# Kernel optimization log

Hardware: AMD Instinct MI355X
Metric: run time of the kernel (lower is better)

The kernel has to match this reference:

```python
import jax, jax.numpy as jnp
import numpy as np

B, CQ, CKV, H, W = 4, 128, 256, 64, 64
NUM_HEADS = 8
SCALE = (CQ // NUM_HEADS) ** (-0.5)


def setup_inputs() -> dict:
    key = jax.random.key(0)
    ks = jax.random.split(key, 10)
    s = 0.02
    return {
        "x_q": jax.random.normal(ks[0], (B, CQ, H, W), dtype=jnp.float32),
        "x_kv": jax.random.normal(ks[1], (B, CKV, H, W), dtype=jnp.float32),
        "Wq": jax.random.normal(ks[2], (CQ, CQ), dtype=jnp.float32) * s,
        "bq": jnp.zeros((CQ,), dtype=jnp.float32),
        "Wk": jax.random.normal(ks[3], (CQ, CKV), dtype=jnp.float32) * s,
        "bk": jnp.zeros((CQ,), dtype=jnp.float32),
        "Wv": jax.random.normal(ks[4], (CQ, CKV), dtype=jnp.float32) * s,
        "bv": jnp.zeros((CQ,), dtype=jnp.float32),
        "Wo": jax.random.normal(ks[5], (CQ, CQ), dtype=jnp.float32) * s,
        "bo": jnp.zeros((CQ,), dtype=jnp.float32),
    }


def _conv1x1(x, Wm, bv_):
    # 1x1 conv == channel-mixing matmul: [B,C,H,W] x [O,C] -> [B,O,H,W]
    return jnp.einsum('bchw,oc->bohw', x, Wm) + bv_[:, None, None]


def reference(x_q, x_kv, Wq, bq, Wk, bk, Wv, bv, Wo, bo):
    b, c, h, w = x_q.shape
    n = h * w
    Q = _conv1x1(x_q, Wq, bq).reshape(b, c, n)   # [B,C,N]
    K = _conv1x1(x_kv, Wk, bk).reshape(b, c, n)  # [B,C,N]
    V = _conv1x1(x_kv, Wv, bv).reshape(b, c, n)  # [B,C,N]
    # attn = softmax(Q^T K * scale) over keys: [B,N,N]
    attn = jax.nn.softmax(jnp.einsum('bcn,bcm->bnm', Q, K) * SCALE, axis=-1)
    out = jnp.einsum('bnm,bcm->bcn', attn, V).reshape(b, c, h, w)
    out = _conv1x1(out, Wo, bo) + x_q
    return out
```

## Files before the change

kernel.cpp:

```cpp
#include <hip/hip_runtime.h>
#include <hip/hip_bf16.h>

typedef __bf16 bf16x8 __attribute__((ext_vector_type(8)));
typedef float f32x4 __attribute__((ext_vector_type(4)));
typedef float f32x16 __attribute__((ext_vector_type(16)));

#define MFMA16(a, b, c) __builtin_amdgcn_mfma_f32_16x16x32_bf16(a, b, c, 0, 0, 0)
#define MFMA32(a, b, c) __builtin_amdgcn_mfma_f32_32x32x16_bf16(a, b, c, 0, 0, 0)

static constexpr int NSP = 4096;
static constexpr float SCALE_L2E = 0.25f * 1.4426950408889634f;

__device__ __forceinline__ bf16x8 ld_frag(const void* p) {
  int4 v = *(const int4*)p;
  return __builtin_bit_cast(bf16x8, v);
}

__device__ __forceinline__ unsigned pk2(float a, float b) {
  unsigned short x = __builtin_bit_cast(unsigned short, (__bf16)a);
  unsigned short y = __builtin_bit_cast(unsigned short, (__bf16)b);
  return (unsigned)x | ((unsigned)y << 16);
}

__device__ __forceinline__ void load_lds16(const void* g, void* l) {
  __builtin_amdgcn_global_load_lds(
      (const __attribute__((address_space(1))) unsigned*)g,
      (__attribute__((address_space(3))) unsigned*)l, 16, 0, 0);
}

__global__ void k_prep(const float* __restrict__ Wq, const float* __restrict__ bq,
                       const float* __restrict__ Wk, const float* __restrict__ Wv,
                       const float* __restrict__ Wo,
                       __bf16* __restrict__ wqb, __bf16* __restrict__ wkb,
                       __bf16* __restrict__ wvb, __bf16* __restrict__ wob,
                       float* __restrict__ bqs) {
  int i = blockIdx.x * 256 + threadIdx.x;
  if (i < 16384)      wqb[i]          = (__bf16)(Wq[i] * SCALE_L2E);
  else if (i < 49152) wkb[i - 16384]  = (__bf16)Wk[i - 16384];
  else if (i < 81920) wvb[i - 49152]  = (__bf16)Wv[i - 49152];
  else if (i < 98304) wob[i - 81920]  = (__bf16)Wo[i - 81920];
  if (i < 128) bqs[i] = bq[i] * SCALE_L2E;
}

template <bool SWZ>
__device__ __forceinline__ void store_tile_T(char* myt, const f32x4* acc, int g, int r,
                                             __bf16* dst_base) {
#pragma unroll
  for (int oc = 0; oc < 8; ++oc) {
#pragma unroll
    for (int rr = 0; rr < 4; ++rr) {
      int o = oc * 16 + g * 4 + rr;
      int byte = (r << 8) + (((o << 1)) ^ (r << 4));
      *(__bf16*)(myt + byte) = (__bf16)acc[oc][rr];
    }
  }
  int l = g * 16 + r;
#pragma unroll
  for (int p = 0; p < 4; ++p) {
    int u = p * 64 + l, row = u >> 4, seg = u & 15;
    int byte = (row << 8) + (seg << 4);
    if (!SWZ) byte ^= (row & 15) << 4;
    int4 v = *(int4*)(myt + byte);
    *(int4*)(dst_base + row * 128 + seg * 8) = v;
  }
}

__global__ __launch_bounds__(256) void k_proj(const float* __restrict__ xq,
                                              const float* __restrict__ xkv,
                                              const __bf16* __restrict__ wqb,
                                              const __bf16* __restrict__ wkb,
                                              const __bf16* __restrict__ wvb,
                                              const float* __restrict__ bqs,
                                              const float* __restrict__ bk,
                                              const float* __restrict__ bv,
                                              __bf16* __restrict__ Qt,
                                              __bf16* __restrict__ Kt,
                                              __bf16* __restrict__ Vm) {
  const int t = threadIdx.x, w = t >> 6, l = t & 63, r = l & 15, g = l >> 4;
  __shared__ __align__(16) char lds[16384];
  char* myt = lds + (w << 12);

  if (blockIdx.x < 256) {
    const int b = blockIdx.x >> 6;
    const int n0 = (blockIdx.x & 63) << 6;
    const int nl = n0 + (w << 4) + r;
    const float* xb = xq + ((size_t)b << 19);
    bf16x8 bx[4];
#pragma unroll
    for (int cc = 0; cc < 4; ++cc) {
#pragma unroll
      for (int i = 0; i < 8; ++i) {
        int c = cc * 32 + g * 8 + i;
        bx[cc][i] = (__bf16)xb[c * 4096 + nl];
      }
    }
    f32x4 acc[8];
#pragma unroll
    for (int oc = 0; oc < 8; ++oc)
#pragma unroll
      for (int rr = 0; rr < 4; ++rr) acc[oc][rr] = bqs[oc * 16 + g * 4 + rr];
#pragma unroll
    for (int oc = 0; oc < 8; ++oc) {
#pragma unroll
      for (int cc = 0; cc < 4; ++cc) {
        bf16x8 a = ld_frag(wqb + (oc * 16 + r) * 128 + cc * 32 + g * 8);
        acc[oc] = MFMA16(a, bx[cc], acc[oc]);
      }
    }
    store_tile_T<false>(myt, acc, g, r, Qt + ((size_t)(b * NSP + n0 + w * 16)) * 128);
  } else {
    const int bid = blockIdx.x - 256;
    const int b = bid >> 6;
    const int n0 = (bid & 63) << 6;
    const int nl = n0 + (w << 4) + r;
    const float* xb = xkv + ((size_t)b << 20);
    bf16x8 bx[8];
#pragma unroll
    for (int cc = 0; cc < 8; ++cc) {
#pragma unroll
      for (int i = 0; i < 8; ++i) {
        int c = cc * 32 + g * 8 + i;
        bx[cc][i] = (__bf16)xb[(size_t)c * 4096 + nl];
      }
    }
    f32x4 acc[8];
#pragma unroll
    for (int oc = 0; oc < 8; ++oc)
#pragma unroll
      for (int rr = 0; rr < 4; ++rr) acc[oc][rr] = bk[oc * 16 + g * 4 + rr];
#pragma unroll
    for (int oc = 0; oc < 8; ++oc) {
#pragma unroll
      for (int cc = 0; cc < 8; ++cc) {
        bf16x8 a = ld_frag(wkb + (oc * 16 + r) * 256 + cc * 32 + g * 8);
        acc[oc] = MFMA16(a, bx[cc], acc[oc]);
      }
    }
    store_tile_T<true>(myt, acc, g, r, Kt + ((size_t)(b * NSP + n0 + w * 16)) * 128);

    f32x4 av[8];
#pragma unroll
    for (int oc = 0; oc < 8; ++oc)
#pragma unroll
      for (int rr = 0; rr < 4; ++rr) av[oc][rr] = bv[oc * 16 + g * 4 + rr];
#pragma unroll
    for (int oc = 0; oc < 8; ++oc) {
#pragma unroll
      for (int cc = 0; cc < 8; ++cc) {
        bf16x8 a = ld_frag(wvb + (oc * 16 + r) * 256 + cc * 32 + g * 8);
        av[oc] = MFMA16(a, bx[cc], av[oc]);
      }
    }
#pragma unroll
    for (int oc = 0; oc < 8; ++oc) {
#pragma unroll
      for (int rr = 0; rr < 4; ++rr) {
        int o = oc * 16 + g * 4 + rr;
        Vm[((size_t)(b * 128 + o) << 12) + (nl ^ ((o & 3) << 3))] = (__bf16)av[oc][rr];
      }
    }
  }
}

template <int SPLIT>
__global__ __launch_bounds__(256, 3) void k_flash(const __bf16* __restrict__ Qt,
                                                  const __bf16* __restrict__ Kt,
                                                  const __bf16* __restrict__ Vm,
                                                  __bf16* __restrict__ Op,
                                                  float2* __restrict__ Ml) {
  const int bid = blockIdx.x;
  const int combo = bid & (4 * SPLIT - 1), qtile = bid / (4 * SPLIT);
  const int b = combo & 3, ks = combo >> 2;
  const int q0 = qtile << 7;
  const int NK = NSP / SPLIT;
  const int t = threadIdx.x, w = t >> 6, l = t & 63;
  const int q31 = l & 31, hi = l >> 5;
  const int swz = (q31 & 15) << 4;
  const int swzV = (q31 & 3) << 4;

  __shared__ __align__(16) char kl[2][8192];
  __shared__ __align__(16) char vl[2][8192];

  const int qA = q0 + w * 32 + q31;
  const __bf16* qp = Qt + ((size_t)(b * NSP + qA)) * 128;
  bf16x8 qf[8];
#pragma unroll
  for (int cc = 0; cc < 8; ++cc) qf[cc] = ld_frag(qp + cc * 16 + hi * 8);

  f32x16 acc[4];
#pragma unroll
  for (int c = 0; c < 4; ++c)
#pragma unroll
    for (int i = 0; i < 16; ++i) acc[c][i] = 0.f;
  f32x4 lp = (f32x4){0.f, 0.f, 0.f, 0.f};

  const char* kbase = (const char*)(Kt + ((size_t)(b * NSP) + ks * NK) * 128);
  const char* vbase = (const char*)(Vm + (size_t)b * 128 * NSP + ks * NK);

  auto STAGE = [&](int bi, int tt) {
#pragma unroll
    for (int i = 0; i < 2; ++i) {
      int u = i * 256 + t;
      load_lds16(kbase + tt * 8192 + u * 16, &kl[bi][u * 16]);
    }
#pragma unroll
    for (int i = 0; i < 2; ++i) {
      int u = i * 256 + t, ch = u >> 2, ko = u & 3;
      load_lds16(vbase + (size_t)ch * 8192 + tt * 64 + ko * 16, &vl[bi][u * 16]);
    }
  };

  STAGE(0, 0);

  const int nit = NK / 32;
  for (int it = 0; it < nit; ++it) {
    const int cur = it & 1;
    asm volatile("s_barrier" ::: "memory");
    if (it + 1 < nit) {
      STAGE(cur ^ 1, it + 1);
      asm volatile("s_waitcnt vmcnt(4)" ::: "memory");
    } else {
      asm volatile("s_waitcnt vmcnt(0)" ::: "memory");
    }
    __builtin_amdgcn_sched_barrier(0);
    asm volatile("s_barrier" ::: "memory");

    const char* kt = kl[cur];
    f32x16 sX = {}, sY = {};
    __builtin_amdgcn_s_setprio(1);
#pragma unroll
    for (int cc = 0; cc < 4; ++cc) {
      bf16x8 kf0 = ld_frag(kt + (q31 << 8) + ((cc * 32 + hi * 16) ^ swz));
      bf16x8 kf1 = ld_frag(kt + (q31 << 8) + (((cc + 4) * 32 + hi * 16) ^ swz));
      sX = MFMA32(kf0, qf[cc], sX);
      sY = MFMA32(kf1, qf[cc + 4], sY);
    }
    __builtin_amdgcn_s_setprio(0);
    f32x16 s;
#pragma unroll
    for (int i = 0; i < 16; ++i) s[i] = sX[i] + sY[i];

#pragma unroll
    for (int i = 0; i < 16; ++i) s[i] = exp2f(s[i]);
#pragma unroll
    for (int i = 0; i < 16; ++i) lp[i & 3] += s[i];

    unsigned pA[4][2], rA[4][2];
#pragma unroll
    for (int q4 = 0; q4 < 4; ++q4) {
      pA[q4][0] = pk2(s[4 * q4 + 0], s[4 * q4 + 1]);
      pA[q4][1] = pk2(s[4 * q4 + 2], s[4 * q4 + 3]);
    }
#pragma unroll
    for (int q4 = 0; q4 < 4; ++q4) {
      rA[q4][0] = __shfl_xor(pA[q4][0], 32);
      rA[q4][1] = __shfl_xor(pA[q4][1], 32);
    }

    const char* vt = vl[cur];
    __builtin_amdgcn_s_setprio(1);
#pragma unroll
    for (int kb = 0; kb < 2; ++kb) {
      uint4 fa;
      fa.x = hi ? rA[2 * kb + 1][0] : pA[2 * kb][0];
      fa.y = hi ? rA[2 * kb + 1][1] : pA[2 * kb][1];
      fa.z = hi ? pA[2 * kb + 1][0] : rA[2 * kb][0];
      fa.w = hi ? pA[2 * kb + 1][1] : rA[2 * kb][1];
      bf16x8 pf = __builtin_bit_cast(bf16x8, fa);
#pragma unroll
      for (int cht = 0; cht < 4; ++cht) {
        bf16x8 vf = ld_frag(vt + (cht * 32 + q31) * 64 + ((kb * 32 + hi * 16) ^ swzV));
        acc[cht] = MFMA32(vf, pf, acc[cht]);
      }
    }
    __builtin_amdgcn_s_setprio(0);
  }

  float lsum = (lp[0] + lp[1]) + (lp[2] + lp[3]);
  lsum += __shfl_xor(lsum, 32);

  const size_t rowA = (size_t)((ks * 4 + b) * NSP + qA) * 128;
#pragma unroll
  for (int cht = 0; cht < 4; ++cht) {
#pragma unroll
    for (int qq = 0; qq < 4; ++qq) {
      uint2 va;
      va.x = pk2(acc[cht][4 * qq + 0], acc[cht][4 * qq + 1]);
      va.y = pk2(acc[cht][4 * qq + 2], acc[cht][4 * qq + 3]);
      *(uint2*)(Op + rowA + cht * 32 + qq * 8 + hi * 4) = va;
    }
  }
  if (hi == 0) {
    Ml[(size_t)(ks * 4 + b) * NSP + qA] = make_float2(0.f, lsum);
  }
}

template <int SPLIT>
__global__ __launch_bounds__(256) void k_oproj(const __bf16* __restrict__ Op,
                                               const float2* __restrict__ Ml,
                                               const __bf16* __restrict__ wob,
                                               const float* __restrict__ bo,
                                               const float* __restrict__ xq,
                                               float* __restrict__ out) {
  const int b = blockIdx.x >> 6;
  const int n0 = (blockIdx.x & 63) << 6;
  const int t = threadIdx.x, w = t >> 6, l = t & 63, r = l & 15, g = l >> 4;
  const int nl = n0 + (w << 4) + r;

  float den = 0.f;
#pragma unroll
  for (int s = 0; s < SPLIT; ++s) den += Ml[(size_t)(s * 4 + b) * NSP + nl].y;
  float inv = 1.f / den;

  bf16x8 bfr[4];
#pragma unroll
  for (int cc = 0; cc < 4; ++cc) {
    float a8[8];
#pragma unroll
    for (int j = 0; j < 8; ++j) a8[j] = 0.f;
#pragma unroll
    for (int s = 0; s < SPLIT; ++s) {
      bf16x8 a = ld_frag(Op + ((size_t)(s * 4 + b) * NSP + nl) * 128 + cc * 32 + g * 8);
#pragma unroll
      for (int j = 0; j < 8; ++j) a8[j] += (float)a[j];
    }
#pragma unroll
    for (int j = 0; j < 8; ++j) bfr[cc][j] = (__bf16)(a8[j] * inv);
  }

  f32x4 acc[8];
#pragma unroll
  for (int oc = 0; oc < 8; ++oc)
#pragma unroll
    for (int rr = 0; rr < 4; ++rr) acc[oc][rr] = bo[oc * 16 + g * 4 + rr];
#pragma unroll
  for (int oc = 0; oc < 8; ++oc) {
#pragma unroll
    for (int cc = 0; cc < 4; ++cc) {
      bf16x8 a = ld_frag(wob + (oc * 16 + r) * 128 + cc * 32 + g * 8);
      acc[oc] = MFMA16(a, bfr[cc], acc[oc]);
    }
  }
#pragma unroll
  for (int oc = 0; oc < 8; ++oc) {
#pragma unroll
    for (int rr = 0; rr < 4; ++rr) {
      int o = oc * 16 + g * 4 + rr;
      size_t idx = ((size_t)(b * 128 + o) << 12) + nl;
      out[idx] = acc[oc][rr] + xq[idx];
    }
  }
}

extern "C" void kernel_launch(void* const* d_in, const int* in_sizes, int n_in,
                              void* d_out, int out_size, void* d_ws, size_t ws_size,
                              hipStream_t stream) {
  const float* xq = (const float*)d_in[0];
  const float* xkv = (const float*)d_in[1];
  const float* Wq = (const float*)d_in[2];
  const float* bq = (const float*)d_in[3];
  const float* Wk = (const float*)d_in[4];
  const float* bk = (const float*)d_in[5];
  const float* Wv = (const float*)d_in[6];
  const float* bv = (const float*)d_in[7];
  const float* Wo = (const float*)d_in[8];
  const float* bo = (const float*)d_in[9];
  float* out = (float*)d_out;

  char* ws = (char*)d_ws;
  __bf16* wqb = (__bf16*)(ws);
  __bf16* wkb = (__bf16*)(ws + 32768);
  __bf16* wvb = (__bf16*)(ws + 98304);
  __bf16* wob = (__bf16*)(ws + 163840);
  float* bqs = (float*)(ws + 196608);
  __bf16* Qt = (__bf16*)(ws + 197120);
  __bf16* Kt = (__bf16*)(ws + 197120 + 4194304);
  __bf16* Vm = (__bf16*)(ws + 197120 + 2 * 4194304);
  __bf16* Op = (__bf16*)(ws + 197120 + 3 * 4194304);
  float2* Ml = (float2*)(ws + 197120 + 3 * 4194304 + 33554432);

  k_prep<<<dim3(384), dim3(256), 0, stream>>>(Wq, bq, Wk, Wv, Wo, wqb, wkb, wvb, wob, bqs);
  k_proj<<<dim3(512), dim3(256), 0, stream>>>(xq, xkv, wqb, wkb, wvb, bqs, bk, bv,
                                              Qt, Kt, Vm);

  const size_t base = 197120ull + 3ull * 4194304;
  const size_t need8 = base + 33554432ull + 1048576ull;
  const size_t need4 = base + 16777216ull + 524288ull;
  if (ws_size >= need8) {
    k_flash<8><<<dim3(1024), dim3(256), 0, stream>>>(Qt, Kt, Vm, Op, Ml);
    k_oproj<8><<<dim3(256), dim3(256), 0, stream>>>(Op, Ml, wob, bo, xq, out);
  } else if (ws_size >= need4) {
    float2* Ml4 = (float2*)(ws + base + 16777216);
    k_flash<4><<<dim3(512), dim3(256), 0, stream>>>(Qt, Kt, Vm, Op, Ml4);
    k_oproj<4><<<dim3(256), dim3(256), 0, stream>>>(Op, Ml4, wob, bo, xq, out);
  } else {
    float2* Ml2 = (float2*)(ws + base + 8388608);
    k_flash<2><<<dim3(256), dim3(256), 0, stream>>>(Qt, Kt, Vm, Op, Ml2);
    k_oproj<2><<<dim3(256), dim3(256), 0, stream>>>(Op, Ml2, wob, bo, xq, out);
  }
}
```

Before: 102.0 us.

## Defer PV MFMAs one iteration and change V LDS swizzle

```diff
diff --git a/kernel.cpp b/kernel.cpp
--- a/kernel.cpp
+++ b/kernel.cpp
@@ -156,7 +156,7 @@
 #pragma unroll
       for (int rr = 0; rr < 4; ++rr) {
         int o = oc * 16 + g * 4 + rr;
-        Vm[((size_t)(b * 128 + o) << 12) + (nl ^ ((o & 3) << 3))] = (__bf16)av[oc][rr];
+        Vm[((size_t)(b * 128 + o) << 12) + (nl ^ (((o >> 1) & 3) << 3))] = (__bf16)av[oc][rr];
       }
     }
   }
@@ -176,7 +176,7 @@
   const int t = threadIdx.x, w = t >> 6, l = t & 63;
   const int q31 = l & 31, hi = l >> 5;
   const int swz = (q31 & 15) << 4;
-  const int swzV = (q31 & 3) << 4;
+  const int swzV = ((q31 >> 1) & 3) << 4;
 
   __shared__ __align__(16) char kl[2][8192];
   __shared__ __align__(16) char vl[2][8192];
@@ -212,17 +212,12 @@
 
   STAGE(0, 0);
 
+  uint4 pfA4 = {}, pfB4 = {};
+
   const int nit = NK / 32;
   for (int it = 0; it < nit; ++it) {
     const int cur = it & 1;
-    asm volatile("s_barrier" ::: "memory");
-    if (it + 1 < nit) {
-      STAGE(cur ^ 1, it + 1);
-      asm volatile("s_waitcnt vmcnt(4)" ::: "memory");
-    } else {
-      asm volatile("s_waitcnt vmcnt(0)" ::: "memory");
-    }
-    __builtin_amdgcn_sched_barrier(0);
+    asm volatile("s_waitcnt vmcnt(0)" ::: "memory");
     asm volatile("s_barrier" ::: "memory");
 
     const char* kt = kl[cur];
@@ -235,11 +230,24 @@
       sX = MFMA32(kf0, qf[cc], sX);
       sY = MFMA32(kf1, qf[cc + 4], sY);
     }
+
+    if (it > 0) {
+      const char* vt = vl[cur ^ 1];
+      bf16x8 pfA = __builtin_bit_cast(bf16x8, pfA4);
+      bf16x8 pfB = __builtin_bit_cast(bf16x8, pfB4);
+#pragma unroll
+      for (int cht = 0; cht < 4; ++cht) {
+        bf16x8 vf0 = ld_frag(vt + (cht * 32 + q31) * 64 + ((hi * 16) ^ swzV));
+        bf16x8 vf1 = ld_frag(vt + (cht * 32 + q31) * 64 + ((32 + hi * 16) ^ swzV));
+        acc[cht] = MFMA32(vf0, pfA, acc[cht]);
+        acc[cht] = MFMA32(vf1, pfB, acc[cht]);
+      }
+    }
     __builtin_amdgcn_s_setprio(0);
+
     f32x16 s;
 #pragma unroll
     for (int i = 0; i < 16; ++i) s[i] = sX[i] + sY[i];
-
 #pragma unroll
     for (int i = 0; i < 16; ++i) s[i] = exp2f(s[i]);
 #pragma unroll
@@ -256,24 +264,30 @@
       rA[q4][0] = __shfl_xor(pA[q4][0], 32);
       rA[q4][1] = __shfl_xor(pA[q4][1], 32);
     }
-
-    const char* vt = vl[cur];
-    __builtin_amdgcn_s_setprio(1);
-#pragma unroll
-    for (int kb = 0; kb < 2; ++kb) {
-      uint4 fa;
-      fa.x = hi ? rA[2 * kb + 1][0] : pA[2 * kb][0];
-      fa.y = hi ? rA[2 * kb + 1][1] : pA[2 * kb][1];
-      fa.z = hi ? pA[2 * kb + 1][0] : rA[2 * kb][0];
-      fa.w = hi ? pA[2 * kb + 1][1] : rA[2 * kb][1];
-      bf16x8 pf = __builtin_bit_cast(bf16x8, fa);
-#pragma unroll
-      for (int cht = 0; cht < 4; ++cht) {
-        bf16x8 vf = ld_frag(vt + (cht * 32 + q31) * 64 + ((kb * 32 + hi * 16) ^ swzV));
-        acc[cht] = MFMA32(vf, pf, acc[cht]);
-      }
-    }
-    __builtin_amdgcn_s_setprio(0);
+    pfA4.x = hi ? rA[1][0] : pA[0][0];
+    pfA4.y = hi ? rA[1][1] : pA[0][1];
+    pfA4.z = hi ? pA[1][0] : rA[0][0];
+    pfA4.w = hi ? pA[1][1] : rA[0][1];
+    pfB4.x = hi ? rA[3][0] : pA[2][0];
+    pfB4.y = hi ? rA[3][1] : pA[2][1];
+    pfB4.z = hi ? pA[3][0] : rA[2][0];
+    pfB4.w = hi ? pA[3][1] : rA[2][1];
+
+    asm volatile("s_barrier" ::: "memory");
+    if (it + 1 < nit) STAGE(cur ^ 1, it + 1);
+  }
+
+  {
+    const char* vt = vl[(nit - 1) & 1];
+    bf16x8 pfA = __builtin_bit_cast(bf16x8, pfA4);
+    bf16x8 pfB = __builtin_bit_cast(bf16x8, pfB4);
+#pragma unroll
+    for (int cht = 0; cht < 4; ++cht) {
+      bf16x8 vf0 = ld_frag(vt + (cht * 32 + q31) * 64 + ((hi * 16) ^ swzV));
+      bf16x8 vf1 = ld_frag(vt + (cht * 32 + q31) * 64 + ((32 + hi * 16) ^ swzV));
+      acc[cht] = MFMA32(vf0, pfA, acc[cht]);
+      acc[cht] = MFMA32(vf1, pfB, acc[cht]);
+    }
   }
 
   float lsum = (lp[0] + lp[1]) + (lp[2] + lp[3]);
```

Result: slower. 107.0 us (+4.9%).
